# Optimization experiments

Hardware: AMD Instinct MI355X
Metric: run time of the kernel (lower is better)

## Reference

```python
import jax, jax.numpy as jnp
import numpy as np

L, E, D, H, HD, DFF = 15, 1024, 1024, 32, 32, 1536
SC, SH, SG, SEQ, B = 32, 256, 256, 64, 128
ALPHA = (2.0 * L) ** (-0.25)


def setup_inputs() -> dict:
    keys = iter(jax.random.split(jax.random.key(0), 40))
    def rn(shape, s=0.02):
        return jax.random.normal(next(keys), shape, jnp.float32) * s
    inp = {"x": jax.random.normal(next(keys), (B, SEQ, E), jnp.float32)}
    inp.update(
        wq_w=rn((L, E, D)), wq_b=rn((L, D)),
        wk_w=rn((L, E, D)), wk_b=rn((L, D)),
        wv_w=rn((L, E, D)), wv_b=rn((L, D)),
        wo_w=rn((L, D, E)), wo_b=rn((L, E)),
        sc_w=rn((L, E, SC)),
        sh1_w=rn((L, SEQ * SC, SH)), sh1_b=rn((L, SH)),
        sln1_g=jnp.ones((L, SH)), sln1_b=jnp.zeros((L, SH)),
        sgf_w=rn((L, SH, H * SG)), sgf_b=rn((L, H * SG)),
        sln2_g=jnp.ones((L, H * SG)), sln2_b=jnp.zeros((L, H * SG)),
        swg_w=rn((L, SG, SEQ * SEQ)),
        ffn1_w=rn((L, E, DFF)), ffn1_b=rn((L, DFF)),
        ffn2_w=rn((L, DFF, E)), ffn2_b=rn((L, E)),
        n1_g=jnp.ones((L, E)), n1_b=jnp.zeros((L, E)),
        n2_g=jnp.ones((L, E)), n2_b=jnp.zeros((L, E)),
    )
    return inp


def _ln(x, g, b, eps=1e-3):
    m = jnp.mean(x, -1, keepdims=True)
    v = jnp.mean((x - m) ** 2, -1, keepdims=True)
    return (x - m) * jax.lax.rsqrt(v + eps) * g + b


def _mish(x):
    return x * jnp.tanh(jax.nn.softplus(x))


def _encoder_layer(x, p):
    (wq_w, wq_b, wk_w, wk_b, wv_w, wv_b, wo_w, wo_b, sc_w, sh1_w, sh1_b,
     sln1_g, sln1_b, sgf_w, sgf_b, sln2_g, sln2_b, swg_w,
     ffn1_w, ffn1_b, ffn2_w, ffn2_b, n1_g, n1_b, n2_g, n2_b) = p
    b, l, _ = x.shape
    q = (x @ wq_w + wq_b).reshape(b, l, H, HD)
    k = (x @ wk_w + wk_b).reshape(b, l, H, HD)
    v = (x @ wv_w + wv_b).reshape(b, l, H, HD)
    logits = jnp.einsum('bqhd,bkhd->bhqk', q, k) / jnp.sqrt(jnp.float32(HD))
    # smolgen: dynamic per-head 64x64 bias from compressed board features
    c = (x @ sc_w).reshape(b, l * SC)                       # [B, 2048]
    h = _ln(jax.nn.silu(c @ sh1_w + sh1_b), sln1_g, sln1_b)  # [B, 256]
    g = _ln(jax.nn.silu(h @ sgf_w + sgf_b), sln2_g, sln2_b)  # [B, H*256]
    sw = (g.reshape(b, H, SG) @ swg_w).reshape(b, H, l, l)   # [B, H, 64, 64]
    attn = jax.nn.softmax(logits + sw, axis=-1)
    av = jnp.einsum('bhqk,bkhd->bqhd', attn, v).reshape(b, l, D)
    out1 = _ln(x + (av @ wo_w + wo_b) * ALPHA, n1_g, n1_b)
    f = _mish(out1 @ ffn1_w + ffn1_b) @ ffn2_w + ffn2_b
    return _ln(out1 + f * ALPHA, n2_g, n2_b)


def reference(x, wq_w, wq_b, wk_w, wk_b, wv_w, wv_b, wo_w, wo_b, sc_w,
              sh1_w, sh1_b, sln1_g, sln1_b, sgf_w, sgf_b, sln2_g, sln2_b,
              swg_w, ffn1_w, ffn1_b, ffn2_w, ffn2_b, n1_g, n1_b, n2_g, n2_b):
    params = (wq_w, wq_b, wk_w, wk_b, wv_w, wv_b, wo_w, wo_b, sc_w,
              sh1_w, sh1_b, sln1_g, sln1_b, sgf_w, sgf_b, sln2_g, sln2_b,
              swg_w, ffn1_w, ffn1_b, ffn2_w, ffn2_b, n1_g, n1_b, n2_g, n2_b)
    def body(h, p):
        return _encoder_layer(h, p), None
    out, _ = jax.lax.scan(body, x, params)
    return out
```

## Files before the change

### kernel.cpp

```cpp
#include <hip/hip_runtime.h>
#include <hip/hip_bf16.h>

typedef __attribute__((ext_vector_type(8))) short bf16x8;
typedef __attribute__((ext_vector_type(4))) float f32x4;
typedef __hip_bfloat16 bf16;

#define ALPHA_F 0.42728713f
#define LN_EPS 1e-3f

__device__ __forceinline__ float silu_f(float x) { return x / (1.0f + __expf(-x)); }
__device__ __forceinline__ float mish_f(float x) {
  if (x > 20.0f) return x;
  float t = 1.0f + __expf(x);
  float t2 = t * t;
  return x * (t2 - 1.0f) / (t2 + 1.0f);
}
__device__ __forceinline__ unsigned short f2bfu(float x) {
  bf16 h = __float2bfloat16(x);
  return *(unsigned short*)&h;
}
__device__ __forceinline__ float bfu2f(unsigned short u) {
  unsigned int v = (unsigned int)u << 16;
  return *(float*)&v;
}

#define MFMA16(acc, a, b) \
  (acc) = __builtin_amdgcn_mfma_f32_16x16x32_bf16((a), (b), (acc), 0, 0, 0)

#define GLOAD_LDS16(gp, lp)                                                              \
  __builtin_amdgcn_global_load_lds((__attribute__((address_space(1))) void*)(void*)(gp), \
                                   (__attribute__((address_space(3))) void*)(void*)(lp), \
                                   16, 0, 0)

__global__ __launch_bounds__(256) void transpose_layer(
    const float* __restrict__ wq, const float* __restrict__ wk, const float* __restrict__ wv,
    const float* __restrict__ wo, const float* __restrict__ f1, const float* __restrict__ f2,
    const float* __restrict__ sgf, const float* __restrict__ swg, const float* __restrict__ sh1,
    const float* __restrict__ scw,
    bf16* __restrict__ Wqkv, bf16* __restrict__ Wo, bf16* __restrict__ Wf1,
    bf16* __restrict__ Wf2, bf16* __restrict__ Wsgf, bf16* __restrict__ Wswg,
    bf16* __restrict__ Wsh1, bf16* __restrict__ Wsc) {
  __shared__ float tile[32][33];
  int b = blockIdx.x;
  const float* W;
  bf16* Wt;
  int K, N, tb;
  if (b < 3072) {
    int m = b >> 10;
    W = (m == 0) ? wq : ((m == 1) ? wk : wv);
    Wt = Wqkv + (size_t)m * 1024 * 1024;
    K = 1024; N = 1024; tb = b & 1023;
  } else if (b < 4096)  { W = wo;  Wt = Wo;   K = 1024; N = 1024; tb = b - 3072; }
  else if (b < 5632)    { W = f1;  Wt = Wf1;  K = 1024; N = 1536; tb = b - 4096; }
  else if (b < 7168)    { W = f2;  Wt = Wf2;  K = 1536; N = 1024; tb = b - 5632; }
  else if (b < 9216)    { W = sgf; Wt = Wsgf; K = 256;  N = 8192; tb = b - 7168; }
  else if (b < 10240)   { W = swg; Wt = Wswg; K = 256;  N = 4096; tb = b - 9216; }
  else if (b < 10752)   { W = sh1; Wt = Wsh1; K = 2048; N = 256;  tb = b - 10240; }
  else                  { W = scw; Wt = Wsc;  K = 1024; N = 32;   tb = b - 10752; }
  int ntx = N >> 5;
  int ty_ = tb / ntx, tx_ = tb - ty_ * ntx;
  int nb = tx_ * 32, kb = ty_ * 32;
  int tx = threadIdx.x & 31, ty = threadIdx.x >> 5;
#pragma unroll
  for (int i = 0; i < 4; ++i)
    tile[ty + i * 8][tx] = W[(size_t)(kb + ty + i * 8) * N + nb + tx];
  __syncthreads();
#pragma unroll
  for (int i = 0; i < 4; ++i)
    Wt[(size_t)(nb + ty + i * 8) * K + kb + tx] = __float2bfloat16(tile[tx][ty + i * 8]);
}

__global__ __launch_bounds__(256) void cvt_f32_bf16_k(const float* __restrict__ in,
                                                      bf16* __restrict__ out, long long n) {
  long long i = ((long long)blockIdx.x * 256 + threadIdx.x) * 4;
  if (i + 3 < n) {
    float4 v = *(const float4*)(in + i);
    out[i + 0] = __float2bfloat16(v.x);
    out[i + 1] = __float2bfloat16(v.y);
    out[i + 2] = __float2bfloat16(v.z);
    out[i + 3] = __float2bfloat16(v.w);
  }
}

__global__ __launch_bounds__(256) void pack3_k(const float* __restrict__ a,
                                               const float* __restrict__ b,
                                               const float* __restrict__ c,
                                               float* __restrict__ o) {
  int i = blockIdx.x * 256 + threadIdx.x;
  if (i < 1024) o[i] = a[i];
  else if (i < 2048) o[i] = b[i - 1024];
  else if (i < 3072) o[i] = c[i - 2048];
}

__global__ __launch_bounds__(1) void sentinel_k(float* __restrict__ o) { o[0] = 1.2345e7f; }

template <int BM, int BN, int ACT, bool OUTBF16, bool BIAS>
__global__ __launch_bounds__(256) void gemm_tn(const bf16* __restrict__ A,
                                               const bf16* __restrict__ Bt,
                                               const float* __restrict__ bias,
                                               float* __restrict__ Cf, bf16* __restrict__ Cb,
                                               int M, int N, int K) {
  constexpr int NWC = (BN == 128) ? 2 : 1;
  constexpr int NWR = 4 / NWC;
  constexpr int AR = BM / (16 * NWR);
  constexpr int AC = BN / (16 * NWC);
  __shared__ __align__(128) short As[2][BM * 32];
  __shared__ __align__(128) short Bs[2][BN * 32];
  int t = threadIdx.x;
  int lane = t & 63, wave = t >> 6;
  int nbx = N / BN;
  int nwg = gridDim.x;
  int q = nwg >> 3, r = nwg & 7;
  int xcd = blockIdx.x & 7, lid = blockIdx.x >> 3;
  int swz = (xcd < r ? xcd * (q + 1) : r * (q + 1) + (xcd - r) * q) + lid;
  int by = swz / nbx, bx = swz - by * nbx;
  int m0 = by * BM, n0 = bx * BN;
  int wr = wave / NWC, wc = wave % NWC;
  int fr = lane & 15;
  int fk = (lane >> 4) << 3;

  f32x4 acc[AR][AC] = {};

  int row0 = t >> 2, ko0 = (t & 3) << 3;

  const bf16* Ag0 = A + (size_t)(m0 + row0) * K + ko0;
  const bf16* Ag1 = A + (size_t)(m0 + 64 + row0) * K + ko0;
  const bf16* Bg0 = Bt + (size_t)(n0 + row0) * K + ko0;
  const bf16* Bg1 = Bt + (size_t)(n0 + 64 + row0) * K + ko0;

  auto stageTo = [&](int buf, int k0) {
    GLOAD_LDS16(Ag0 + k0, &As[buf][wave * 512]);
    if constexpr (BM == 128) GLOAD_LDS16(Ag1 + k0, &As[buf][2048 + wave * 512]);
    GLOAD_LDS16(Bg0 + k0, &Bs[buf][wave * 512]);
    if constexpr (BN == 128) GLOAD_LDS16(Bg1 + k0, &Bs[buf][2048 + wave * 512]);
  };

  int nk = K >> 5;
  stageTo(0, 0);
  __syncthreads();

  const int rdA = (wr * (BM / NWR) + fr) * 32 + fk;
  const int rdB = (wc * (BN / NWC) + fr) * 32 + fk;

  for (int kt = 0; kt < nk; ++kt) {
    int cur = kt & 1;
    if (kt + 1 < nk) stageTo(cur ^ 1, (kt + 1) << 5);
    bf16x8 af[AR], bfv[AC];
#pragma unroll
    for (int a = 0; a < AR; ++a) af[a] = *(const bf16x8*)(&As[cur][rdA + a * 512]);
#pragma unroll
    for (int b = 0; b < AC; ++b) bfv[b] = *(const bf16x8*)(&Bs[cur][rdB + b * 512]);
#pragma unroll
    for (int a = 0; a < AR; ++a)
#pragma unroll
      for (int b = 0; b < AC; ++b) MFMA16(acc[a][b], af[a], bfv[b]);
    __syncthreads();
  }
  int lr = (lane >> 4) << 2;
  int lc = lane & 15;
#pragma unroll
  for (int a = 0; a < AR; ++a) {
#pragma unroll
    for (int b = 0; b < AC; ++b) {
      int col = n0 + wc * (BN / NWC) + b * 16 + lc;
      float bv = 0.0f;
      if constexpr (BIAS) bv = bias[col];
#pragma unroll
      for (int j = 0; j < 4; ++j) {
        int rowi = m0 + wr * (BM / NWR) + a * 16 + lr + j;
        float v = acc[a][b][j] + bv;
        if constexpr (ACT == 1) v = silu_f(v);
        if constexpr (ACT == 2) v = mish_f(v);
        if constexpr (OUTBF16) Cb[(size_t)rowi * N + col] = __float2bfloat16(v);
        else Cf[(size_t)rowi * N + col] = v;
      }
    }
  }
}

__global__ __launch_bounds__(64) void c_kernel(const bf16* __restrict__ xb,
                                               const bf16* __restrict__ Wsc,
                                               bf16* __restrict__ cout) {
  const int lane = threadIdx.x;
  const int fr = lane & 15, s4 = lane >> 4;
  const int row0 = blockIdx.x * 16;
  f32x4 acc[2] = {};
  const bf16* Arow = xb + (size_t)(row0 + fr) * 1024 + s4 * 8;
  const bf16* B0 = Wsc + (size_t)fr * 1024 + s4 * 8;
  const bf16* B1 = Wsc + (size_t)(16 + fr) * 1024 + s4 * 8;
#pragma unroll 8
  for (int kt = 0; kt < 32; ++kt) {
    bf16x8 a = *(const bf16x8*)(Arow + kt * 32);
    bf16x8 b0 = *(const bf16x8*)(B0 + kt * 32);
    bf16x8 b1 = *(const bf16x8*)(B1 + kt * 32);
    acc[0] = __builtin_amdgcn_mfma_f32_16x16x32_bf16(a, b0, acc[0], 0, 0, 0);
    acc[1] = __builtin_amdgcn_mfma_f32_16x16x32_bf16(a, b1, acc[1], 0, 0, 0);
  }
#pragma unroll
  for (int n2 = 0; n2 < 2; ++n2)
#pragma unroll
    for (int j = 0; j < 4; ++j)
      cout[(size_t)(row0 + s4 * 4 + j) * 32 + n2 * 16 + fr] =
          __float2bfloat16(acc[n2][j]);
}

__global__ __launch_bounds__(256) void ln256_kernel(const float* __restrict__ hpre,
                                                    const float* __restrict__ gam,
                                                    const float* __restrict__ bet,
                                                    bf16* __restrict__ hb) {
  __shared__ float rsm[4], rs2[4], st2[2];
  int t = threadIdx.x, row = blockIdx.x;
  float sv = hpre[(size_t)row * 256 + t];
  float s = sv, s2 = sv * sv;
#pragma unroll
  for (int o = 32; o > 0; o >>= 1) { s += __shfl_down(s, o); s2 += __shfl_down(s2, o); }
  if ((t & 63) == 0) { rsm[t >> 6] = s; rs2[t >> 6] = s2; }
  __syncthreads();
  if (t == 0) {
    float a = rsm[0] + rsm[1] + rsm[2] + rsm[3];
    float b2 = rs2[0] + rs2[1] + rs2[2] + rs2[3];
    float m = a * (1.0f / 256.0f);
    st2[0] = m;
    st2[1] = rsqrtf(b2 * (1.0f / 256.0f) - m * m + LN_EPS);
  }
  __syncthreads();
  float y = (sv - st2[0]) * st2[1] * gam[t] + bet[t];
  hb[(size_t)row * 256 + t] = __float2bfloat16(y);
}

__global__ __launch_bounds__(1024) void ln8192_kernel(const float* __restrict__ gpre,
                                                      const float* __restrict__ gam,
                                                      const float* __restrict__ bet,
                                                      bf16* __restrict__ gb) {
  __shared__ float rsm[16], rs2[16], st2[2];
  int t = threadIdx.x, row = blockIdx.x;
  const float* p = gpre + (size_t)row * 8192;
  float v[8];
  float s = 0.0f, s2 = 0.0f;
#pragma unroll
  for (int i = 0; i < 8; ++i) {
    v[i] = p[t + i * 1024];
    s += v[i];
    s2 += v[i] * v[i];
  }
#pragma unroll
  for (int o = 32; o > 0; o >>= 1) { s += __shfl_down(s, o); s2 += __shfl_down(s2, o); }
  int lane = t & 63, w = t >> 6;
  if (lane == 0) { rsm[w] = s; rs2[w] = s2; }
  __syncthreads();
  if (t == 0) {
    float a = 0.0f, b2 = 0.0f;
#pragma unroll
    for (int i = 0; i < 16; ++i) { a += rsm[i]; b2 += rs2[i]; }
    float m = a * (1.0f / 8192.0f);
    st2[0] = m;
    st2[1] = rsqrtf(b2 * (1.0f / 8192.0f) - m * m + LN_EPS);
  }
  __syncthreads();
  float m = st2[0], r = st2[1];
#pragma unroll
  for (int i = 0; i < 8; ++i) {
    int n = t + i * 1024;
    gb[(size_t)row * 8192 + n] = __float2bfloat16((v[i] - m) * r * gam[n] + bet[n]);
  }
}

__global__ __launch_bounds__(256) void ln_residual_kernel(const float* __restrict__ base,
                                                          const bf16* __restrict__ delta,
                                                          const float* __restrict__ gam,
                                                          const float* __restrict__ bet,
                                                          float* __restrict__ outf,
                                                          bf16* __restrict__ outb) {
  __shared__ float rsm[4], rs2[4], st2[2];
  int t = threadIdx.x, row = blockIdx.x;
  float4 bv = ((const float4*)(base + (size_t)row * 1024))[t];
  ushort4 du = ((const ushort4*)(delta + (size_t)row * 1024))[t];
  float4 v;
  v.x = bv.x + bfu2f(du.x) * ALPHA_F;
  v.y = bv.y + bfu2f(du.y) * ALPHA_F;
  v.z = bv.z + bfu2f(du.z) * ALPHA_F;
  v.w = bv.w + bfu2f(du.w) * ALPHA_F;
  float s = v.x + v.y + v.z + v.w;
  float s2 = v.x * v.x + v.y * v.y + v.z * v.z + v.w * v.w;
#pragma unroll
  for (int o = 32; o > 0; o >>= 1) { s += __shfl_down(s, o); s2 += __shfl_down(s2, o); }
  if ((t & 63) == 0) { rsm[t >> 6] = s; rs2[t >> 6] = s2; }
  __syncthreads();
  if (t == 0) {
    float a = rsm[0] + rsm[1] + rsm[2] + rsm[3];
    float b2 = rs2[0] + rs2[1] + rs2[2] + rs2[3];
    float m = a * (1.0f / 1024.0f);
    st2[0] = m;
    st2[1] = rsqrtf(b2 * (1.0f / 1024.0f) - m * m + LN_EPS);
  }
  __syncthreads();
  float m = st2[0], r = st2[1];
  float4 g4 = ((const float4*)gam)[t];
  float4 b4 = ((const float4*)bet)[t];
  float4 y;
  y.x = (v.x - m) * r * g4.x + b4.x;
  y.y = (v.y - m) * r * g4.y + b4.y;
  y.z = (v.z - m) * r * g4.z + b4.z;
  y.w = (v.w - m) * r * g4.w + b4.w;
  ((float4*)(outf + (size_t)row * 1024))[t] = y;
  ushort4 o4;
  o4.x = f2bfu(y.x); o4.y = f2bfu(y.y); o4.z = f2bfu(y.z); o4.w = f2bfu(y.w);
  ((ushort4*)(outb + (size_t)row * 1024))[t] = o4;
}

__global__ __launch_bounds__(256) void attn_kernel(const bf16* __restrict__ qkv,
                                                   const bf16* __restrict__ sw,
                                                   bf16* __restrict__ avb) {
  __shared__ __align__(16) short Vt[32 * 72];
  __shared__ __align__(16) short Sw[64 * 64];
  __shared__ __align__(16) short Pl[64 * 72];
  const int t = threadIdx.x, lane = t & 63, w = t >> 6;
  const int fr = lane & 15, s4 = lane >> 4;
  const int bh = blockIdx.x, b = bh >> 5, h = bh & 31;
  const size_t qb = (size_t)b * 64 * 3072 + h * 32;
  {
    int k = t >> 2, d0 = (t & 3) * 8;
    bf16x8 v = *(const bf16x8*)(qkv + qb + (size_t)k * 3072 + 2048 + d0);
#pragma unroll
    for (int i = 0; i < 8; ++i) Vt[(d0 + i) * 72 + k] = v[i];
  }
  {
    const bf16* swp = sw + (size_t)bh * 4096;
    *(bf16x8*)(Sw + t * 8) = *(const bf16x8*)(swp + t * 8);
    *(bf16x8*)(Sw + 2048 + t * 8) = *(const bf16x8*)(swp + 2048 + t * 8);
  }
  __syncthreads();
  f32x4 acc[4] = {};
  {
    bf16x8 aq = *(const bf16x8*)(qkv + qb + (size_t)(16 * w + fr) * 3072 + s4 * 8);
#pragma unroll
    for (int n = 0; n < 4; ++n) {
      bf16x8 bk = *(const bf16x8*)(qkv + qb + (size_t)(n * 16 + fr) * 3072 + 1024 + s4 * 8);
      acc[n] = __builtin_amdgcn_mfma_f32_16x16x32_bf16(aq, bk, acc[n], 0, 0, 0);
    }
  }
  float rinv[4];
#pragma unroll
  for (int j = 0; j < 4; ++j) {
    int q = 16 * w + s4 * 4 + j;
    float pv[4];
    float mx = -1e30f;
#pragma unroll
    for (int n = 0; n < 4; ++n) {
      float v = acc[n][j] * 0.17677669529663687f +
                __bfloat162float(((const bf16*)Sw)[q * 64 + n * 16 + fr]);
      pv[n] = v;
      mx = fmaxf(mx, v);
    }
    mx = fmaxf(mx, __shfl_xor(mx, 1));
    mx = fmaxf(mx, __shfl_xor(mx, 2));
    mx = fmaxf(mx, __shfl_xor(mx, 4));
    mx = fmaxf(mx, __shfl_xor(mx, 8));
    float sum = 0.0f;
#pragma unroll
    for (int n = 0; n < 4; ++n) {
      float e = __expf(pv[n] - mx);
      sum += e;
      ((bf16*)Pl)[q * 72 + n * 16 + fr] = __float2bfloat16(e);
    }
    sum += __shfl_xor(sum, 1);
    sum += __shfl_xor(sum, 2);
    sum += __shfl_xor(sum, 4);
    sum += __shfl_xor(sum, 8);
    rinv[j] = 1.0f / sum;
  }
  __syncthreads();
  f32x4 acc2[2] = {};
#pragma unroll
  for (int kt = 0; kt < 2; ++kt) {
    bf16x8 ap = *(const bf16x8*)(Pl + (16 * w + fr) * 72 + kt * 32 + s4 * 8);
#pragma unroll
    for (int n2 = 0; n2 < 2; ++n2) {
      bf16x8 bv = *(const bf16x8*)(Vt + (n2 * 16 + fr) * 72 + kt * 32 + s4 * 8);
      acc2[n2] = __builtin_amdgcn_mfma_f32_16x16x32_bf16(ap, bv, acc2[n2], 0, 0, 0);
    }
  }
#pragma unroll
  for (int n2 = 0; n2 < 2; ++n2) {
#pragma unroll
    for (int j = 0; j < 4; ++j) {
      int q = 16 * w + s4 * 4 + j;
      int d = n2 * 16 + fr;
      avb[(size_t)(b * 64 + q) * 1024 + h * 32 + d] =
          __float2bfloat16(acc2[n2][j] * rinv[j]);
    }
  }
}

extern "C" void kernel_launch(void* const* d_in, const int* in_sizes, int n_in,
                              void* d_out, int out_size, void* d_ws, size_t ws_size,
                              hipStream_t stream) {
  const float* x_in   = (const float*)d_in[0];
  const float* wq_w   = (const float*)d_in[1];
  const float* wq_b   = (const float*)d_in[2];
  const float* wk_w   = (const float*)d_in[3];
  const float* wk_b   = (const float*)d_in[4];
  const float* wv_w   = (const float*)d_in[5];
  const float* wv_b   = (const float*)d_in[6];
  const float* wo_w   = (const float*)d_in[7];
  const float* wo_b   = (const float*)d_in[8];
  const float* sc_w   = (const float*)d_in[9];
  const float* sh1_w  = (const float*)d_in[10];
  const float* sh1_b  = (const float*)d_in[11];
  const float* sln1_g = (const float*)d_in[12];
  const float* sln1_b = (const float*)d_in[13];
  const float* sgf_w  = (const float*)d_in[14];
  const float* sgf_b  = (const float*)d_in[15];
  const float* sln2_g = (const float*)d_in[16];
  const float* sln2_b = (const float*)d_in[17];
  const float* swg_w  = (const float*)d_in[18];
  const float* ffn1_w = (const float*)d_in[19];
  const float* ffn1_b = (const float*)d_in[20];
  const float* ffn2_w = (const float*)d_in[21];
  const float* ffn2_b = (const float*)d_in[22];
  const float* n1_g   = (const float*)d_in[23];
  const float* n1_b   = (const float*)d_in[24];
  const float* n2_g   = (const float*)d_in[25];
  const float* n2_b   = (const float*)d_in[26];

  char* ws = (char*)d_ws;
  size_t off = 0;
  auto alloc = [&](size_t bytes) -> void* {
    void* p = ws + off;
    off += (bytes + 255) & ~(size_t)255;
    return p;
  };
  bf16*  xb    = (bf16*)alloc(8192ULL * 1024 * 2);
  float* P0    = (float*)alloc(8192ULL * 1024 * 4);
  float* P1    = (float*)alloc(8192ULL * 1024 * 4);
  bf16*  dT    = (bf16*)alloc(8192ULL * 1024 * 2);
  bf16*  Wqkv  = (bf16*)alloc(3072ULL * 1024 * 2);
  float* bqkv  = (float*)alloc(3072ULL * 4);
  bf16*  Wo    = (bf16*)alloc(1024ULL * 1024 * 2);
  bf16*  Wf1   = (bf16*)alloc(1536ULL * 1024 * 2);
  bf16*  Wf2   = (bf16*)alloc(1024ULL * 1536 * 2);
  bf16*  Wsgf  = (bf16*)alloc(8192ULL * 256 * 2);
  bf16*  Wswg  = (bf16*)alloc(4096ULL * 256 * 2);
  bf16*  Wsh1  = (bf16*)alloc(256ULL * 2048 * 2);
  bf16*  Wsc   = (bf16*)alloc(32ULL * 1024 * 2);
  bf16*  qkvb  = (bf16*)alloc(8192ULL * 3072 * 2);
  bf16*  cbuf  = (bf16*)alloc(8192ULL * 32 * 2);
  float* hpre  = (float*)alloc(128ULL * 256 * 4);
  bf16*  hbb   = (bf16*)alloc(128ULL * 256 * 2);
  float* gpre  = (float*)alloc(128ULL * 8192 * 4);
  bf16*  gbb   = (bf16*)alloc(128ULL * 8192 * 2);
  bf16*  swb   = (bf16*)alloc(4096ULL * 4096 * 2);
  bf16*  avb   = (bf16*)alloc(8192ULL * 1024 * 2);
  bf16*  out1b = (bf16*)alloc(8192ULL * 1024 * 2);
  bf16*  f1b   = (bf16*)alloc(8192ULL * 1536 * 2);
  if (off > ws_size) {
    sentinel_k<<<1, 1, 0, stream>>>((float*)d_out);
    return;
  }

  cvt_f32_bf16_k<<<8192, 256, 0, stream>>>(x_in, xb, 8192LL * 1024);

  for (int l = 0; l < 15; ++l) {
    const float* wq   = wq_w + (size_t)l * 1024 * 1024;
    const float* wk   = wk_w + (size_t)l * 1024 * 1024;
    const float* wv   = wv_w + (size_t)l * 1024 * 1024;
    const float* wo   = wo_w + (size_t)l * 1024 * 1024;
    const float* f1w  = ffn1_w + (size_t)l * 1024 * 1536;
    const float* f2w  = ffn2_w + (size_t)l * 1536 * 1024;
    const float* sgf  = sgf_w + (size_t)l * 256 * 8192;
    const float* swg  = swg_w + (size_t)l * 256 * 4096;
    const float* scw  = sc_w + (size_t)l * 1024 * 32;
    const float* sh1w = sh1_w + (size_t)l * 2048 * 256;

    transpose_layer<<<10784, 256, 0, stream>>>(wq, wk, wv, wo, f1w, f2w, sgf, swg, sh1w, scw,
                                               Wqkv, Wo, Wf1, Wf2, Wsgf, Wswg, Wsh1, Wsc);
    pack3_k<<<12, 256, 0, stream>>>(wq_b + l * 1024, wk_b + l * 1024, wv_b + l * 1024, bqkv);

    const float* xc = (l == 0) ? x_in : ((l & 1) ? P0 : P1);
    float* Pout = (l & 1) ? P1 : P0;

    gemm_tn<128, 128, 0, true, true><<<1536, 256, 0, stream>>>(xb, Wqkv, bqkv, nullptr, qkvb,
                                                               8192, 3072, 1024);
    c_kernel<<<512, 64, 0, stream>>>(xb, Wsc, cbuf);
    gemm_tn<64, 64, 1, false, true><<<8, 256, 0, stream>>>(cbuf, Wsh1, sh1_b + l * 256,
                                                           hpre, nullptr, 128, 256, 2048);
    ln256_kernel<<<128, 256, 0, stream>>>(hpre, sln1_g + l * 256, sln1_b + l * 256, hbb);
    gemm_tn<64, 64, 1, false, true><<<256, 256, 0, stream>>>(hbb, Wsgf,
                                                             sgf_b + (size_t)l * 8192,
                                                             gpre, nullptr, 128, 8192, 256);
    ln8192_kernel<<<128, 1024, 0, stream>>>(gpre, sln2_g + (size_t)l * 8192,
                                            sln2_b + (size_t)l * 8192, gbb);
    gemm_tn<64, 64, 0, true, false><<<4096, 256, 0, stream>>>(gbb, Wswg, nullptr, nullptr, swb,
                                                              4096, 4096, 256);
    attn_kernel<<<4096, 256, 0, stream>>>(qkvb, swb, avb);
    gemm_tn<64, 64, 0, true, true><<<2048, 256, 0, stream>>>(avb, Wo, wo_b + l * 1024,
                                                             nullptr, dT, 8192, 1024, 1024);
    ln_residual_kernel<<<8192, 256, 0, stream>>>(xc, dT, n1_g + l * 1024, n1_b + l * 1024,
                                                 Pout, out1b);
    gemm_tn<64, 64, 2, true, true><<<3072, 256, 0, stream>>>(out1b, Wf1, ffn1_b + l * 1536,
                                                             nullptr, f1b, 8192, 1536, 1024);
    gemm_tn<64, 64, 0, true, true><<<2048, 256, 0, stream>>>(f1b, Wf2, ffn2_b + l * 1024,
                                                             nullptr, dT, 8192, 1024, 1536);
    float* xnext = (l == 14) ? (float*)d_out : Pout;
    ln_residual_kernel<<<8192, 256, 0, stream>>>(Pout, dT, n2_g + l * 1024, n2_b + l * 1024,
                                                 xnext, xb);
  }
}
```

Before: 5.435 ms.

## Fuse QKV GEMM, smolgen compress and next-layer weight transpose into one kernel

Replaces the per-layer transpose, bias pack, QKV GEMM and c_kernel launches with a single megaA kernel. Its block ranges compute QKV, compute the smolgen compression, and transpose the next layer's weights into a double-buffered set, so that conversion overlaps current-layer work. The smolgen sh1 GEMM, both layernorms and the sgf GEMM are fused into one 128-block smolgen_mid kernel, and attention now reads the smolgen bias straight from global memory instead of staging it in LDS. This cuts launches and intermediate round-trips at the cost of double the weight buffer memory and a smolgen_mid with low parallelism doing scalar dot products.

```diff
diff --git a/kernel.cpp b/kernel.cpp
--- a/kernel.cpp
+++ b/kernel.cpp
@@ -32,42 +32,61 @@
                                    (__attribute__((address_space(3))) void*)(void*)(lp), \
                                    16, 0, 0)
 
-__global__ __launch_bounds__(256) void transpose_layer(
-    const float* __restrict__ wq, const float* __restrict__ wk, const float* __restrict__ wv,
-    const float* __restrict__ wo, const float* __restrict__ f1, const float* __restrict__ f2,
-    const float* __restrict__ sgf, const float* __restrict__ swg, const float* __restrict__ sh1,
-    const float* __restrict__ scw,
-    bf16* __restrict__ Wqkv, bf16* __restrict__ Wo, bf16* __restrict__ Wf1,
-    bf16* __restrict__ Wf2, bf16* __restrict__ Wsgf, bf16* __restrict__ Wswg,
-    bf16* __restrict__ Wsh1, bf16* __restrict__ Wsc) {
-  __shared__ float tile[32][33];
-  int b = blockIdx.x;
+__global__ __launch_bounds__(1) void sentinel_k(float* __restrict__ o) { o[0] = 1.2345e7f; }
+
+__device__ __forceinline__ void transpose_body(
+    int tb, float* tile ,
+    const float* wq, const float* wk, const float* wv, const float* wo,
+    const float* f1, const float* f2, const float* sgf, const float* swg,
+    const float* sh1, const float* scw,
+    const float* bq, const float* bk, const float* bv,
+    bf16* Wqkv, bf16* Wo, bf16* Wf1, bf16* Wf2, bf16* Wsgf, bf16* Wswg,
+    bf16* Wsh1, bf16* Wsc, float* bqkv) {
+  if (tb >= 10784) {
+    int i = (tb - 10784) * 256 + threadIdx.x;
+    if (i < 1024) bqkv[i] = bq[i];
+    else if (i < 2048) bqkv[i] = bk[i - 1024];
+    else bqkv[i] = bv[i - 2048];
+    return;
+  }
   const float* W;
   bf16* Wt;
-  int K, N, tb;
-  if (b < 3072) {
-    int m = b >> 10;
+  int K, N, b2;
+  if (tb < 3072) {
+    int m = tb >> 10;
     W = (m == 0) ? wq : ((m == 1) ? wk : wv);
     Wt = Wqkv + (size_t)m * 1024 * 1024;
-    K = 1024; N = 1024; tb = b & 1023;
-  } else if (b < 4096)  { W = wo;  Wt = Wo;   K = 1024; N = 1024; tb = b - 3072; }
-  else if (b < 5632)    { W = f1;  Wt = Wf1;  K = 1024; N = 1536; tb = b - 4096; }
-  else if (b < 7168)    { W = f2;  Wt = Wf2;  K = 1536; N = 1024; tb = b - 5632; }
-  else if (b < 9216)    { W = sgf; Wt = Wsgf; K = 256;  N = 8192; tb = b - 7168; }
-  else if (b < 10240)   { W = swg; Wt = Wswg; K = 256;  N = 4096; tb = b - 9216; }
-  else if (b < 10752)   { W = sh1; Wt = Wsh1; K = 2048; N = 256;  tb = b - 10240; }
-  else                  { W = scw; Wt = Wsc;  K = 1024; N = 32;   tb = b - 10752; }
+    K = 1024; N = 1024; b2 = tb & 1023;
+  } else if (tb < 4096)  { W = wo;  Wt = Wo;   K = 1024; N = 1024; b2 = tb - 3072; }
+  else if (tb < 5632)    { W = f1;  Wt = Wf1;  K = 1024; N = 1536; b2 = tb - 4096; }
+  else if (tb < 7168)    { W = f2;  Wt = Wf2;  K = 1536; N = 1024; b2 = tb - 5632; }
+  else if (tb < 9216)    { W = sgf; Wt = Wsgf; K = 256;  N = 8192; b2 = tb - 7168; }
+  else if (tb < 10240)   { W = swg; Wt = Wswg; K = 256;  N = 4096; b2 = tb - 9216; }
+  else if (tb < 10752)   { W = sh1; Wt = Wsh1; K = 2048; N = 256;  b2 = tb - 10240; }
+  else                   { W = scw; Wt = Wsc;  K = 1024; N = 32;   b2 = tb - 10752; }
   int ntx = N >> 5;
-  int ty_ = tb / ntx, tx_ = tb - ty_ * ntx;
+  int ty_ = b2 / ntx, tx_ = b2 - ty_ * ntx;
   int nb = tx_ * 32, kb = ty_ * 32;
   int tx = threadIdx.x & 31, ty = threadIdx.x >> 5;
 #pragma unroll
   for (int i = 0; i < 4; ++i)
-    tile[ty + i * 8][tx] = W[(size_t)(kb + ty + i * 8) * N + nb + tx];
+    tile[(ty + i * 8) * 33 + tx] = W[(size_t)(kb + ty + i * 8) * N + nb + tx];
   __syncthreads();
 #pragma unroll
   for (int i = 0; i < 4; ++i)
-    Wt[(size_t)(nb + ty + i * 8) * K + kb + tx] = __float2bfloat16(tile[tx][ty + i * 8]);
+    Wt[(size_t)(nb + ty + i * 8) * K + kb + tx] = __float2bfloat16(tile[tx * 33 + ty + i * 8]);
+}
+
+__global__ __launch_bounds__(256) void transpose_layer(
+    const float* wq, const float* wk, const float* wv, const float* wo,
+    const float* f1, const float* f2, const float* sgf, const float* swg,
+    const float* sh1, const float* scw,
+    const float* bq, const float* bk, const float* bv,
+    bf16* Wqkv, bf16* Wo, bf16* Wf1, bf16* Wf2, bf16* Wsgf, bf16* Wswg,
+    bf16* Wsh1, bf16* Wsc, float* bqkv) {
+  __shared__ float tile[32 * 33];
+  transpose_body(blockIdx.x, tile, wq, wk, wv, wo, f1, f2, sgf, swg, sh1, scw,
+                 bq, bk, bv, Wqkv, Wo, Wf1, Wf2, Wsgf, Wswg, Wsh1, Wsc, bqkv);
 }
 
 __global__ __launch_bounds__(256) void cvt_f32_bf16_k(const float* __restrict__ in,
@@ -82,17 +101,104 @@
   }
 }
 
-__global__ __launch_bounds__(256) void pack3_k(const float* __restrict__ a,
-                                               const float* __restrict__ b,
-                                               const float* __restrict__ c,
-                                               float* __restrict__ o) {
-  int i = blockIdx.x * 256 + threadIdx.x;
-  if (i < 1024) o[i] = a[i];
-  else if (i < 2048) o[i] = b[i - 1024];
-  else if (i < 3072) o[i] = c[i - 2048];
-}
-
-__global__ __launch_bounds__(1) void sentinel_k(float* __restrict__ o) { o[0] = 1.2345e7f; }
+__global__ __launch_bounds__(256) void megaA(
+    const bf16* __restrict__ xb,
+    const bf16* __restrict__ Wqkv, const float* __restrict__ bqkv,
+    bf16* __restrict__ qkvb,
+    const bf16* __restrict__ Wsc, bf16* __restrict__ cbuf,
+    int doT,
+    const float* wq, const float* wk, const float* wv, const float* wo,
+    const float* f1, const float* f2, const float* sgf, const float* swg,
+    const float* sh1, const float* scw,
+    const float* bq, const float* bk, const float* bv,
+    bf16* WqkvN, bf16* WoN, bf16* Wf1N, bf16* Wf2N, bf16* WsgfN, bf16* WswgN,
+    bf16* Wsh1N, bf16* WscN, float* bqkvN) {
+  __shared__ __align__(128) short LB[16384];
+  const int bid = blockIdx.x;
+  const int t = threadIdx.x;
+  if (bid < 1536) {
+    const int lane = t & 63, wave = t >> 6;
+    int xcd = bid & 7, lid = bid >> 3;
+    int swz = xcd * 192 + lid;
+    int by = swz / 24, bx = swz - by * 24;
+    int m0 = by << 7, n0 = bx << 7;
+    int wr = wave >> 1, wc = wave & 1;
+    int fr = lane & 15, fk = (lane >> 4) << 3;
+    f32x4 acc[4][4] = {};
+    int row0 = t >> 2, ko0 = (t & 3) << 3;
+    const bf16* Ag0 = xb + (size_t)(m0 + row0) * 1024 + ko0;
+    const bf16* Ag1 = xb + (size_t)(m0 + 64 + row0) * 1024 + ko0;
+    const bf16* Bg0 = Wqkv + (size_t)(n0 + row0) * 1024 + ko0;
+    const bf16* Bg1 = Wqkv + (size_t)(n0 + 64 + row0) * 1024 + ko0;
+    auto stageTo = [&](int buf, int k0) {
+      short* Asb = LB + buf * 4096;
+      short* Bsb = LB + 8192 + buf * 4096;
+      GLOAD_LDS16(Ag0 + k0, Asb + wave * 512);
+      GLOAD_LDS16(Ag1 + k0, Asb + 2048 + wave * 512);
+      GLOAD_LDS16(Bg0 + k0, Bsb + wave * 512);
+      GLOAD_LDS16(Bg1 + k0, Bsb + 2048 + wave * 512);
+    };
+    stageTo(0, 0);
+    __syncthreads();
+    const int rdA = (wr * 64 + fr) * 32 + fk;
+    const int rdB = (wc * 64 + fr) * 32 + fk;
+    for (int kt = 0; kt < 32; ++kt) {
+      int cur = kt & 1;
+      if (kt + 1 < 32) stageTo(cur ^ 1, (kt + 1) << 5);
+      const short* Asb = LB + cur * 4096;
+      const short* Bsb = LB + 8192 + cur * 4096;
+      bf16x8 af[4], bfv[4];
+#pragma unroll
+      for (int a = 0; a < 4; ++a) af[a] = *(const bf16x8*)(Asb + rdA + a * 512);
+#pragma unroll
+      for (int b = 0; b < 4; ++b) bfv[b] = *(const bf16x8*)(Bsb + rdB + b * 512);
+#pragma unroll
+      for (int a = 0; a < 4; ++a)
+#pragma unroll
+        for (int b = 0; b < 4; ++b) MFMA16(acc[a][b], af[a], bfv[b]);
+      __syncthreads();
+    }
+    int lr = (lane >> 4) << 2, lc = lane & 15;
+#pragma unroll
+    for (int a = 0; a < 4; ++a)
+#pragma unroll
+      for (int b = 0; b < 4; ++b) {
+        int col = n0 + wc * 64 + b * 16 + lc;
+        float bv = bqkv[col];
+#pragma unroll
+        for (int j = 0; j < 4; ++j) {
+          int rowi = m0 + wr * 64 + a * 16 + lr + j;
+          qkvb[(size_t)rowi * 3072 + col] = __float2bfloat16(acc[a][b][j] + bv);
+        }
+      }
+  } else if (bid < 1664) {
+    const int lane = t & 63, w = t >> 6;
+    const int fr = lane & 15, s4 = lane >> 4;
+    const int row0 = ((bid - 1536) * 4 + w) * 16;
+    f32x4 acc[2] = {};
+    const bf16* Arow = xb + (size_t)(row0 + fr) * 1024 + s4 * 8;
+    const bf16* B0 = Wsc + (size_t)fr * 1024 + s4 * 8;
+    const bf16* B1 = Wsc + (size_t)(16 + fr) * 1024 + s4 * 8;
+#pragma unroll 8
+    for (int kt = 0; kt < 32; ++kt) {
+      bf16x8 a = *(const bf16x8*)(Arow + kt * 32);
+      bf16x8 b0 = *(const bf16x8*)(B0 + kt * 32);
+      bf16x8 b1 = *(const bf16x8*)(B1 + kt * 32);
+      acc[0] = __builtin_amdgcn_mfma_f32_16x16x32_bf16(a, b0, acc[0], 0, 0, 0);
+      acc[1] = __builtin_amdgcn_mfma_f32_16x16x32_bf16(a, b1, acc[1], 0, 0, 0);
+    }
+#pragma unroll
+    for (int n2 = 0; n2 < 2; ++n2)
+#pragma unroll
+      for (int j = 0; j < 4; ++j)
+        cbuf[(size_t)(row0 + s4 * 4 + j) * 32 + n2 * 16 + fr] =
+            __float2bfloat16(acc[n2][j]);
+  } else {
+    if (!doT) return;
+    transpose_body(bid - 1664, (float*)LB, wq, wk, wv, wo, f1, f2, sgf, swg, sh1, scw,
+                   bq, bk, bv, WqkvN, WoN, Wf1N, Wf2N, WsgfN, WswgN, Wsh1N, WscN, bqkvN);
+  }
+}
 
 template <int BM, int BN, int ACT, bool OUTBF16, bool BIAS>
 __global__ __launch_bounds__(256) void gemm_tn(const bf16* __restrict__ A,
@@ -178,90 +284,93 @@
   }
 }
 
-__global__ __launch_bounds__(64) void c_kernel(const bf16* __restrict__ xb,
-                                               const bf16* __restrict__ Wsc,
-                                               bf16* __restrict__ cout) {
-  const int lane = threadIdx.x;
-  const int fr = lane & 15, s4 = lane >> 4;
-  const int row0 = blockIdx.x * 16;
-  f32x4 acc[2] = {};
-  const bf16* Arow = xb + (size_t)(row0 + fr) * 1024 + s4 * 8;
-  const bf16* B0 = Wsc + (size_t)fr * 1024 + s4 * 8;
-  const bf16* B1 = Wsc + (size_t)(16 + fr) * 1024 + s4 * 8;
-#pragma unroll 8
-  for (int kt = 0; kt < 32; ++kt) {
-    bf16x8 a = *(const bf16x8*)(Arow + kt * 32);
-    bf16x8 b0 = *(const bf16x8*)(B0 + kt * 32);
-    bf16x8 b1 = *(const bf16x8*)(B1 + kt * 32);
-    acc[0] = __builtin_amdgcn_mfma_f32_16x16x32_bf16(a, b0, acc[0], 0, 0, 0);
-    acc[1] = __builtin_amdgcn_mfma_f32_16x16x32_bf16(a, b1, acc[1], 0, 0, 0);
-  }
-#pragma unroll
-  for (int n2 = 0; n2 < 2; ++n2)
-#pragma unroll
-    for (int j = 0; j < 4; ++j)
-      cout[(size_t)(row0 + s4 * 4 + j) * 32 + n2 * 16 + fr] =
-          __float2bfloat16(acc[n2][j]);
-}
-
-__global__ __launch_bounds__(256) void ln256_kernel(const float* __restrict__ hpre,
-                                                    const float* __restrict__ gam,
-                                                    const float* __restrict__ bet,
-                                                    bf16* __restrict__ hb) {
+__global__ __launch_bounds__(256) void smolgen_mid(
+    const bf16* __restrict__ cbuf, const bf16* __restrict__ Wsh1,
+    const float* __restrict__ sh1b, const float* __restrict__ g1,
+    const float* __restrict__ b1,
+    const bf16* __restrict__ Wsgf, const float* __restrict__ sgfb,
+    const float* __restrict__ g2, const float* __restrict__ b2,
+    bf16* __restrict__ gbb) {
+  __shared__ short cs[2048];
+  __shared__ short hs[256];
   __shared__ float rsm[4], rs2[4], st2[2];
-  int t = threadIdx.x, row = blockIdx.x;
-  float sv = hpre[(size_t)row * 256 + t];
-  float s = sv, s2 = sv * sv;
+  const int t = threadIdx.x, r = blockIdx.x;
+  *(bf16x8*)(cs + t * 8) = *(const bf16x8*)(cbuf + (size_t)r * 2048 + t * 8);
+  __syncthreads();
+  float a0 = sh1b[t], a1 = 0.0f;
+  const bf16* wr1 = Wsh1 + (size_t)t * 2048;
+  for (int k = 0; k < 2048; k += 16) {
+    bf16x8 w8 = *(const bf16x8*)(wr1 + k);
+    bf16x8 c8 = *(const bf16x8*)(cs + k);
+    bf16x8 w8b = *(const bf16x8*)(wr1 + k + 8);
+    bf16x8 c8b = *(const bf16x8*)(cs + k + 8);
+#pragma unroll
+    for (int j = 0; j < 8; ++j) {
+      a0 += bfu2f((unsigned short)c8[j]) * bfu2f((unsigned short)w8[j]);
+      a1 += bfu2f((unsigned short)c8b[j]) * bfu2f((unsigned short)w8b[j]);
+    }
+  }
+  float sv = silu_f(a0 + a1);
+  {
+    float s = sv, s2 = sv * sv;
+#pragma unroll
+    for (int o = 32; o > 0; o >>= 1) { s += __shfl_down(s, o); s2 += __shfl_down(s2, o); }
+    if ((t & 63) == 0) { rsm[t >> 6] = s; rs2[t >> 6] = s2; }
+    __syncthreads();
+    if (t == 0) {
+      float a = rsm[0] + rsm[1] + rsm[2] + rsm[3];
+      float bb = rs2[0] + rs2[1] + rs2[2] + rs2[3];
+      float m = a * (1.0f / 256.0f);
+      st2[0] = m;
+      st2[1] = rsqrtf(bb * (1.0f / 256.0f) - m * m + LN_EPS);
+    }
+    __syncthreads();
+    float y = (sv - st2[0]) * st2[1] * g1[t] + b1[t];
+    hs[t] = (short)f2bfu(y);
+  }
+  __syncthreads();
+  float gs[32];
+  float s = 0.0f, s2 = 0.0f;
+#pragma unroll
+  for (int i = 0; i < 32; ++i) {
+    int n = t + i * 256;
+    float p0 = sgfb[n], p1 = 0.0f;
+    const bf16* wr2 = Wsgf + (size_t)n * 256;
+#pragma unroll 4
+    for (int k = 0; k < 256; k += 16) {
+      bf16x8 w8 = *(const bf16x8*)(wr2 + k);
+      bf16x8 h8 = *(const bf16x8*)(hs + k);
+      bf16x8 w8b = *(const bf16x8*)(wr2 + k + 8);
+      bf16x8 h8b = *(const bf16x8*)(hs + k + 8);
+#pragma unroll
+      for (int j = 0; j < 8; ++j) {
+        p0 += bfu2f((unsigned short)h8[j]) * bfu2f((unsigned short)w8[j]);
+        p1 += bfu2f((unsigned short)h8b[j]) * bfu2f((unsigned short)w8b[j]);
+      }
+    }
+    float gv = silu_f(p0 + p1);
+    gs[i] = gv;
+    s += gv;
+    s2 += gv * gv;
+  }
+  __syncthreads();
 #pragma unroll
   for (int o = 32; o > 0; o >>= 1) { s += __shfl_down(s, o); s2 += __shfl_down(s2, o); }
   if ((t & 63) == 0) { rsm[t >> 6] = s; rs2[t >> 6] = s2; }
   __syncthreads();
   if (t == 0) {
     float a = rsm[0] + rsm[1] + rsm[2] + rsm[3];
-    float b2 = rs2[0] + rs2[1] + rs2[2] + rs2[3];
-    float m = a * (1.0f / 256.0f);
-    st2[0] = m;
-    st2[1] = rsqrtf(b2 * (1.0f / 256.0f) - m * m + LN_EPS);
-  }
-  __syncthreads();
-  float y = (sv - st2[0]) * st2[1] * gam[t] + bet[t];
-  hb[(size_t)row * 256 + t] = __float2bfloat16(y);
-}
-
-__global__ __launch_bounds__(1024) void ln8192_kernel(const float* __restrict__ gpre,
-                                                      const float* __restrict__ gam,
-                                                      const float* __restrict__ bet,
-                                                      bf16* __restrict__ gb) {
-  __shared__ float rsm[16], rs2[16], st2[2];
-  int t = threadIdx.x, row = blockIdx.x;
-  const float* p = gpre + (size_t)row * 8192;
-  float v[8];
-  float s = 0.0f, s2 = 0.0f;
-#pragma unroll
-  for (int i = 0; i < 8; ++i) {
-    v[i] = p[t + i * 1024];
-    s += v[i];
-    s2 += v[i] * v[i];
-  }
-#pragma unroll
-  for (int o = 32; o > 0; o >>= 1) { s += __shfl_down(s, o); s2 += __shfl_down(s2, o); }
-  int lane = t & 63, w = t >> 6;
-  if (lane == 0) { rsm[w] = s; rs2[w] = s2; }
-  __syncthreads();
-  if (t == 0) {
-    float a = 0.0f, b2 = 0.0f;
-#pragma unroll
-    for (int i = 0; i < 16; ++i) { a += rsm[i]; b2 += rs2[i]; }
+    float bb = rs2[0] + rs2[1] + rs2[2] + rs2[3];
     float m = a * (1.0f / 8192.0f);
     st2[0] = m;
-    st2[1] = rsqrtf(b2 * (1.0f / 8192.0f) - m * m + LN_EPS);
-  }
-  __syncthreads();
-  float m = st2[0], r = st2[1];
-#pragma unroll
-  for (int i = 0; i < 8; ++i) {
-    int n = t + i * 1024;
-    gb[(size_t)row * 8192 + n] = __float2bfloat16((v[i] - m) * r * gam[n] + bet[n]);
+    st2[1] = rsqrtf(bb * (1.0f / 8192.0f) - m * m + LN_EPS);
+  }
+  __syncthreads();
+  float m = st2[0], rr = st2[1];
+#pragma unroll
+  for (int i = 0; i < 32; ++i) {
+    int n = t + i * 256;
+    gbb[(size_t)r * 8192 + n] = __float2bfloat16((gs[i] - m) * rr * g2[n] + b2[n]);
   }
 }
 
@@ -312,7 +421,6 @@
                                                    const bf16* __restrict__ sw,
                                                    bf16* __restrict__ avb) {
   __shared__ __align__(16) short Vt[32 * 72];
-  __shared__ __align__(16) short Sw[64 * 64];
   __shared__ __align__(16) short Pl[64 * 72];
   const int t = threadIdx.x, lane = t & 63, w = t >> 6;
   const int fr = lane & 15, s4 = lane >> 4;
@@ -324,12 +432,6 @@
 #pragma unroll
     for (int i = 0; i < 8; ++i) Vt[(d0 + i) * 72 + k] = v[i];
   }
-  {
-    const bf16* swp = sw + (size_t)bh * 4096;
-    *(bf16x8*)(Sw + t * 8) = *(const bf16x8*)(swp + t * 8);
-    *(bf16x8*)(Sw + 2048 + t * 8) = *(const bf16x8*)(swp + 2048 + t * 8);
-  }
-  __syncthreads();
   f32x4 acc[4] = {};
   {
     bf16x8 aq = *(const bf16x8*)(qkv + qb + (size_t)(16 * w + fr) * 3072 + s4 * 8);
@@ -339,6 +441,7 @@
       acc[n] = __builtin_amdgcn_mfma_f32_16x16x32_bf16(aq, bk, acc[n], 0, 0, 0);
     }
   }
+  const bf16* swp = sw + (size_t)bh * 4096;
   float rinv[4];
 #pragma unroll
   for (int j = 0; j < 4; ++j) {
@@ -348,7 +451,7 @@
 #pragma unroll
     for (int n = 0; n < 4; ++n) {
       float v = acc[n][j] * 0.17677669529663687f +
-                __bfloat162float(((const bf16*)Sw)[q * 64 + n * 16 + fr]);
+                __bfloat162float(swp[q * 64 + n * 16 + fr]);
       pv[n] = v;
       mx = fmaxf(mx, v);
     }
@@ -434,20 +537,17 @@
   float* P0    = (float*)alloc(8192ULL * 1024 * 4);
   float* P1    = (float*)alloc(8192ULL * 1024 * 4);
   bf16*  dT    = (bf16*)alloc(8192ULL * 1024 * 2);
-  bf16*  Wqkv  = (bf16*)alloc(3072ULL * 1024 * 2);
-  float* bqkv  = (float*)alloc(3072ULL * 4);
-  bf16*  Wo    = (bf16*)alloc(1024ULL * 1024 * 2);
-  bf16*  Wf1   = (bf16*)alloc(1536ULL * 1024 * 2);
-  bf16*  Wf2   = (bf16*)alloc(1024ULL * 1536 * 2);
-  bf16*  Wsgf  = (bf16*)alloc(8192ULL * 256 * 2);
-  bf16*  Wswg  = (bf16*)alloc(4096ULL * 256 * 2);
-  bf16*  Wsh1  = (bf16*)alloc(256ULL * 2048 * 2);
-  bf16*  Wsc   = (bf16*)alloc(32ULL * 1024 * 2);
+  bf16*  WqkvB = (bf16*)alloc(2ULL * 3072 * 1024 * 2);
+  float* bqkvB = (float*)alloc(2ULL * 3072 * 4);
+  bf16*  WoB   = (bf16*)alloc(2ULL * 1024 * 1024 * 2);
+  bf16*  Wf1B  = (bf16*)alloc(2ULL * 1536 * 1024 * 2);
+  bf16*  Wf2B  = (bf16*)alloc(2ULL * 1024 * 1536 * 2);
+  bf16*  WsgfB = (bf16*)alloc(2ULL * 8192 * 256 * 2);
+  bf16*  WswgB = (bf16*)alloc(2ULL * 4096 * 256 * 2);
+  bf16*  Wsh1B = (bf16*)alloc(2ULL * 256 * 2048 * 2);
+  bf16*  WscB  = (bf16*)alloc(2ULL * 32 * 1024 * 2);
   bf16*  qkvb  = (bf16*)alloc(8192ULL * 3072 * 2);
   bf16*  cbuf  = (bf16*)alloc(8192ULL * 32 * 2);
-  float* hpre  = (float*)alloc(128ULL * 256 * 4);
-  bf16*  hbb   = (bf16*)alloc(128ULL * 256 * 2);
-  float* gpre  = (float*)alloc(128ULL * 8192 * 4);
   bf16*  gbb   = (bf16*)alloc(128ULL * 8192 * 2);
   bf16*  swb   = (bf16*)alloc(4096ULL * 4096 * 2);
   bf16*  avb   = (bf16*)alloc(8192ULL * 1024 * 2);
@@ -459,39 +559,47 @@
   }
 
   cvt_f32_bf16_k<<<8192, 256, 0, stream>>>(x_in, xb, 8192LL * 1024);
+  transpose_layer<<<10796, 256, 0, stream>>>(
+      wq_w, wk_w, wv_w, wo_w, ffn1_w, ffn2_w, sgf_w, swg_w, sh1_w, sc_w,
+      wq_b, wk_b, wv_b,
+      WqkvB, WoB, Wf1B, Wf2B, WsgfB, WswgB, Wsh1B, WscB, bqkvB);
 
   for (int l = 0; l < 15; ++l) {
-    const float* wq   = wq_w + (size_t)l * 1024 * 1024;
-    const float* wk   = wk_w + (size_t)l * 1024 * 1024;
-    const float* wv   = wv_w + (size_t)l * 1024 * 1024;
-    const float* wo   = wo_w + (size_t)l * 1024 * 1024;
-    const float* f1w  = ffn1_w + (size_t)l * 1024 * 1536;
-    const float* f2w  = ffn2_w + (size_t)l * 1536 * 1024;
-    const float* sgf  = sgf_w + (size_t)l * 256 * 8192;
-    const float* swg  = swg_w + (size_t)l * 256 * 4096;
-    const float* scw  = sc_w + (size_t)l * 1024 * 32;
-    const float* sh1w = sh1_w + (size_t)l * 2048 * 256;
-
-    transpose_layer<<<10784, 256, 0, stream>>>(wq, wk, wv, wo, f1w, f2w, sgf, swg, sh1w, scw,
-                                               Wqkv, Wo, Wf1, Wf2, Wsgf, Wswg, Wsh1, Wsc);
-    pack3_k<<<12, 256, 0, stream>>>(wq_b + l * 1024, wk_b + l * 1024, wv_b + l * 1024, bqkv);
+    const int cur = l & 1, nxt = cur ^ 1;
+    const int lp = l + 1;
+    bf16*  Wqkv = WqkvB + (size_t)cur * 3072 * 1024;
+    float* bqkv = bqkvB + (size_t)cur * 3072;
+    bf16*  Wo   = WoB   + (size_t)cur * 1024 * 1024;
+    bf16*  Wf1  = Wf1B  + (size_t)cur * 1536 * 1024;
+    bf16*  Wf2  = Wf2B  + (size_t)cur * 1024 * 1536;
+    bf16*  Wsgf = WsgfB + (size_t)cur * 8192 * 256;
+    bf16*  Wswg = WswgB + (size_t)cur * 4096 * 256;
+    bf16*  Wsh1 = Wsh1B + (size_t)cur * 256 * 2048;
+    bf16*  Wsc  = WscB  + (size_t)cur * 32 * 1024;
 
     const float* xc = (l == 0) ? x_in : ((l & 1) ? P0 : P1);
     float* Pout = (l & 1) ? P1 : P0;
 
-    gemm_tn<128, 128, 0, true, true><<<1536, 256, 0, stream>>>(xb, Wqkv, bqkv, nullptr, qkvb,
-                                                               8192, 3072, 1024);
-    c_kernel<<<512, 64, 0, stream>>>(xb, Wsc, cbuf);
-    gemm_tn<64, 64, 1, false, true><<<8, 256, 0, stream>>>(cbuf, Wsh1, sh1_b + l * 256,
-                                                           hpre, nullptr, 128, 256, 2048);
-    ln256_kernel<<<128, 256, 0, stream>>>(hpre, sln1_g + l * 256, sln1_b + l * 256, hbb);
-    gemm_tn<64, 64, 1, false, true><<<256, 256, 0, stream>>>(hbb, Wsgf,
-                                                             sgf_b + (size_t)l * 8192,
-                                                             gpre, nullptr, 128, 8192, 256);
-    ln8192_kernel<<<128, 1024, 0, stream>>>(gpre, sln2_g + (size_t)l * 8192,
-                                            sln2_b + (size_t)l * 8192, gbb);
-    gemm_tn<64, 64, 0, true, false><<<4096, 256, 0, stream>>>(gbb, Wswg, nullptr, nullptr, swb,
-                                                              4096, 4096, 256);
+    megaA<<<12460, 256, 0, stream>>>(
+        xb, Wqkv, bqkv, qkvb, Wsc, cbuf, (l < 14) ? 1 : 0,
+        wq_w + (size_t)lp * 1048576, wk_w + (size_t)lp * 1048576,
+        wv_w + (size_t)lp * 1048576, wo_w + (size_t)lp * 1048576,
+        ffn1_w + (size_t)lp * 1024 * 1536, ffn2_w + (size_t)lp * 1536 * 1024,
+        sgf_w + (size_t)lp * 256 * 8192, swg_w + (size_t)lp * 256 * 4096,
+        sh1_w + (size_t)lp * 2048 * 256, sc_w + (size_t)lp * 1024 * 32,
+        wq_b + (size_t)lp * 1024, wk_b + (size_t)lp * 1024, wv_b + (size_t)lp * 1024,
+        WqkvB + (size_t)nxt * 3072 * 1024, WoB + (size_t)nxt * 1024 * 1024,
+        Wf1B + (size_t)nxt * 1536 * 1024, Wf2B + (size_t)nxt * 1024 * 1536,
+        WsgfB + (size_t)nxt * 8192 * 256, WswgB + (size_t)nxt * 4096 * 256,
+        Wsh1B + (size_t)nxt * 256 * 2048, WscB + (size_t)nxt * 32 * 1024,
+        bqkvB + (size_t)nxt * 3072);
+    smolgen_mid<<<128, 256, 0, stream>>>(cbuf, Wsh1, sh1_b + l * 256,
+                                         sln1_g + l * 256, sln1_b + l * 256,
+                                         Wsgf, sgf_b + (size_t)l * 8192,
+                                         sln2_g + (size_t)l * 8192,
+                                         sln2_b + (size_t)l * 8192, gbb);
+    gemm_tn<64, 64, 0, true, false><<<4096, 256, 0, stream>>>(gbb, Wswg, nullptr, nullptr,
+                                                              swb, 4096, 4096, 256);
     attn_kernel<<<4096, 256, 0, stream>>>(qkvb, swb, avb);
     gemm_tn<64, 64, 0, true, true><<<2048, 256, 0, stream>>>(avb, Wo, wo_b + l * 1024,
                                                              nullptr, dT, 8192, 1024, 1024);
```

Result: slower. 8.108 ms (+49.2%).
